# Kernel optimization log

Measured on AMD Instinct MI355X. Metric: run time of the kernel, lower is better.

The kernel has to match this reference:

```python
import jax, jax.numpy as jnp
import numpy as np

N = 100000
E = 1600000
IN_C = 128
HID = 256
EPS = 1e-5


def setup_inputs() -> dict:
    key = jax.random.key(0)
    ks = jax.random.split(key, 20)
    s = lambda fi, fo: (1.0 / np.sqrt(fi))
    inp = {
        "x": jax.random.normal(ks[0], (N, IN_C), dtype=jnp.float32),
        "edge_index": jax.random.randint(ks[1], (2, E), 0, N, dtype=jnp.int64),
        # SAGEConv (in -> hidden): lin_l (on aggregated neighbors, with bias), lin_r (root, no bias)
        "Wl": jax.random.normal(ks[2], (HID, IN_C), dtype=jnp.float32) * s(IN_C, HID),
        "bl": jnp.zeros((HID,), dtype=jnp.float32),
        "Wr": jax.random.normal(ks[3], (HID, IN_C), dtype=jnp.float32) * s(IN_C, HID),
        # bns[0]
        "bn_g": jnp.ones((HID,), dtype=jnp.float32),
        "bn_b": jnp.zeros((HID,), dtype=jnp.float32),
        # linear stack hidden->hidden->64->14->2
        "W1": jax.random.normal(ks[4], (HID, HID), dtype=jnp.float32) * s(HID, HID),
        "b1": jnp.zeros((HID,), dtype=jnp.float32),
        "W2": jax.random.normal(ks[5], (64, HID), dtype=jnp.float32) * s(HID, 64),
        "b2": jnp.zeros((64,), dtype=jnp.float32),
        "W3": jax.random.normal(ks[6], (14, 64), dtype=jnp.float32) * s(64, 14),
        "b3": jnp.zeros((14,), dtype=jnp.float32),
        "W4": jax.random.normal(ks[7], (2, 14), dtype=jnp.float32) * s(14, 2),
        "b4": jnp.zeros((2,), dtype=jnp.float32),
        # bns2: BN(hidden), BN(64), BN(14)
        "g1": jnp.ones((HID,), dtype=jnp.float32), "bb1": jnp.zeros((HID,), dtype=jnp.float32),
        "g2": jnp.ones((64,), dtype=jnp.float32), "bb2": jnp.zeros((64,), dtype=jnp.float32),
        "g3": jnp.ones((14,), dtype=jnp.float32), "bb3": jnp.zeros((14,), dtype=jnp.float32),
    }
    return inp


def _bn(h, g, b):
    # training-mode BatchNorm1d: batch mean, biased variance
    m = h.mean(axis=0)
    v = jnp.mean((h - m) ** 2, axis=0)
    return g * (h - m) * jax.lax.rsqrt(v + EPS) + b


def _sage_mean(x, edge_index, Wl, bl, Wr):
    src, dst = edge_index[0], edge_index[1]
    n = x.shape[0]
    agg = jax.ops.segment_sum(x[src], dst, num_segments=n)  # [N, F]
    cnt = jax.ops.segment_sum(jnp.ones((src.shape[0],), x.dtype), dst, num_segments=n)
    agg = agg / jnp.maximum(cnt, 1.0)[:, None]
    return agg @ Wl.T + bl + x @ Wr.T


def reference(x, edge_index, Wl, bl, Wr, bn_g, bn_b,
              W1, b1, W2, b2, W3, b3, W4, b4,
              g1, bb1, g2, bb2, g3, bb3):
    # convs2[:-1] loop (num_layers=2 -> single conv), dropout is identity (eval)
    h = _sage_mean(x, edge_index, Wl, bl, Wr)
    h = jax.nn.relu(_bn(h, bn_g, bn_b))
    # linear stack with bns2 + relu
    h = jax.nn.relu(_bn(h @ W1.T + b1, g1, bb1))
    h = jax.nn.relu(_bn(h @ W2.T + b2, g2, bb2))
    h = jax.nn.relu(_bn(h @ W3.T + b3, g3, bb3))
    h = h @ W4.T + b4
    return jax.nn.log_softmax(h, axis=-1)
```

## Files before the change

kernel.cpp:

```cpp
#include <hip/hip_runtime.h>
#include <math.h>

#define BN_EPS 1e-5f
#define STAT_NB 64
#define GBIN 512
#define BSH 7
#define XB 2048

typedef unsigned short u16;
typedef __attribute__((ext_vector_type(8))) unsigned short u16x8;
typedef __attribute__((ext_vector_type(8))) short bf16x8;
typedef __attribute__((ext_vector_type(4))) float f32x4;

__device__ __forceinline__ float bf2f(u16 b){
  union{unsigned int u; float f;} c; c.u = ((unsigned int)b)<<16; return c.f;
}
__device__ __forceinline__ u16 f2bf(float f){
  union{float f; unsigned int u;} c; c.f=f;
  unsigned int u = c.u;
  return (u16)((u + 0x7fffu + ((u>>16)&1u)) >> 16);
}
__device__ __forceinline__ void gl16(const u16* g, u16* l){
  __builtin_amdgcn_global_load_lds((const __attribute__((address_space(1))) void*)g,
                                   (__attribute__((address_space(3))) void*)l, 16, 0, 0);
}

__global__ __launch_bounds__(256) void k_prep(
    const float* __restrict__ Wl, const float* __restrict__ Wr,
    const float* __restrict__ W1, const float* __restrict__ W2,
    const float* __restrict__ x, const int* __restrict__ ei, int E, int nbkt,
    u16* __restrict__ Wb1, u16* __restrict__ Wb2, u16* __restrict__ Wb3,
    u16* __restrict__ Acat, int n, int* __restrict__ blkhist, int* __restrict__ flags){
  __shared__ int hist[1024];
  int bid = blockIdx.x, tid = threadIdx.x;
  auto cv8 = [](const float* s)->u16x8{
    float4 a = ((const float4*)s)[0], b = ((const float4*)s)[1];
    u16x8 v;
    v[0]=f2bf(a.x); v[1]=f2bf(a.y); v[2]=f2bf(a.z); v[3]=f2bf(a.w);
    v[4]=f2bf(b.x); v[5]=f2bf(b.y); v[6]=f2bf(b.z); v[7]=f2bf(b.w);
    return v;
  };
  if (bid < XB){
    int i = bid*256 + tid;
    int total = n*16;
    for (; i<total; i+=XB*256){
      int r = i>>4, kb = (i&15)*8;
      *(u16x8*)(Acat + (size_t)r*256 + 128 + kb) = cv8(x + (size_t)r*128 + kb);
    }
  } else if (bid < XB+512){
    int blk = bid - XB;
    for (int b=tid;b<1024;b+=256) hist[b]=0;
    __syncthreads();
    int per = (E + GBIN - 1)/GBIN;
    int e0 = blk*per, e1 = min(E, e0+per);
    for (int e=e0+tid; e<e1; e+=256)
      atomicAdd(&hist[ei[(size_t)E+e]>>BSH], 1);
    __syncthreads();
    for (int b=tid;b<nbkt;b+=256) blkhist[(size_t)b*GBIN + blk] = hist[b];
  } else {
    int wb = bid - (XB+512);
    if (wb==0 && tid<8) flags[tid]=0;
    if (wb < 32){
      int i = wb*256 + tid;
      int c = i>>5, kb = (i&31)*8;
      const float* src = (kb<128) ? (Wl + (size_t)c*128 + kb) : (Wr + (size_t)c*128 + kb-128);
      *(u16x8*)(Wb1 + (size_t)c*256 + kb) = cv8(src);
    } else if (wb < 64){
      int i = (wb-32)*256 + tid;
      *(u16x8*)(Wb2 + (size_t)i*8) = cv8(W1 + (size_t)i*8);
    } else {
      int i = (wb-64)*256 + tid;
      if (i < 2048) *(u16x8*)(Wb3 + (size_t)i*8) = cv8(W2 + (size_t)i*8);
    }
  }
}

__global__ __launch_bounds__(256) void k_rowscan(int* __restrict__ blkhist, int nbkt,
                                                 int* __restrict__ bbase, int* __restrict__ counter){
  __shared__ int lastFlag;
  __shared__ int ps[256];
  int tid = threadIdx.x;
  int wid = (blockIdx.x*256 + tid) >> 6;
  int lane = tid & 63;
  if (wid < nbkt){
    int* row = blkhist + (size_t)wid*GBIN + lane*8;
    int v[8];
    #pragma unroll
    for (int j=0;j<8;j++) v[j] = row[j];
    int s = 0;
    #pragma unroll
    for (int j=0;j<8;j++){ int t = v[j]; v[j] = s; s += t; }
    int incl = s;
    #pragma unroll
    for (int o=1;o<64;o<<=1){
      int t = __shfl_up(incl, o, 64);
      if (lane >= o) incl += t;
    }
    int excl = incl - s;
    #pragma unroll
    for (int j=0;j<8;j++) row[j] = v[j] + excl;
    if (lane == 63) bbase[wid] = incl;
  }
  __threadfence();
  if (tid==0) lastFlag = (atomicAdd(counter,1) == (int)gridDim.x-1);
  __syncthreads();
  if (!lastFlag) return;
  int base = tid*4;
  int v0 = (base  <nbkt)? bbase[base  ] : 0;
  int v1 = (base+1<nbkt)? bbase[base+1] : 0;
  int v2 = (base+2<nbkt)? bbase[base+2] : 0;
  int v3 = (base+3<nbkt)? bbase[base+3] : 0;
  int run = v0+v1+v2+v3;
  ps[tid] = run;
  __syncthreads();
  #pragma unroll
  for (int o=1;o<256;o<<=1){
    int t = (tid>=o)? ps[tid-o] : 0;
    __syncthreads();
    ps[tid] += t;
    __syncthreads();
  }
  int excl = ps[tid]-run;
  if (base  <nbkt) bbase[base  ] = excl;
  if (base+1<nbkt) bbase[base+1] = excl+v0;
  if (base+2<nbkt) bbase[base+2] = excl+v0+v1;
  if (base+3<nbkt) bbase[base+3] = excl+v0+v1+v2;
  if (tid==255) bbase[nbkt] = ps[255];
}

__global__ __launch_bounds__(256) void k_scatter(const int* __restrict__ ei, int E, int nbkt,
                                                 const int* __restrict__ blkhist,
                                                 const int* __restrict__ bbase,
                                                 int* __restrict__ pairs){
  __shared__ int cur[1024];
  int tid = threadIdx.x, blk = blockIdx.x;
  for (int b=tid;b<nbkt;b+=256) cur[b] = bbase[b] + blkhist[(size_t)b*GBIN + blk];
  __syncthreads();
  int per = (E + GBIN - 1)/GBIN;
  int e0 = blk*per, e1 = min(E, e0+per);
  for (int e=e0+tid; e<e1; e+=256){
    int dst = ei[(size_t)E+e];
    int src = ei[e];
    int b = dst>>BSH;
    int p = atomicAdd(&cur[b], 1);
    pairs[p] = (src<<BSH) | (dst & 127);
  }
}

__global__ __launch_bounds__(256) void k_bucket_csr(const int* __restrict__ pairs,
                                                    const int* __restrict__ bbase,
                                                    int nbkt, int n,
                                                    int2* __restrict__ odeg,
                                                    int* __restrict__ eidx){
  __shared__ int hist[128], loff[128], cur2[128];
  int tid = threadIdx.x, b = blockIdx.x;
  if (b >= nbkt) return;
  int n0 = b<<BSH;
  int nn = min(128, n - n0);
  int e0 = bbase[b], e1 = bbase[b+1];
  int cnt = e1 - e0;
  if (tid<128) hist[tid]=0;
  __syncthreads();
  for (int i=tid;i<cnt;i+=256)
    atomicAdd(&hist[pairs[e0+i] & 127], 1);
  __syncthreads();
  int hv=0;
  if (tid<128){ hv = hist[tid]; loff[tid] = hv; }
  __syncthreads();
  #pragma unroll
  for (int o=1;o<128;o<<=1){
    int t = (tid<128 && tid>=o)? loff[tid-o] : 0;
    __syncthreads();
    if (tid<128) loff[tid]+=t;
    __syncthreads();
  }
  if (tid<128){
    int ex = loff[tid]-hv;
    cur2[tid] = ex;
    if (tid<nn) odeg[n0+tid] = make_int2(e0+ex, hv);
  }
  __syncthreads();
  for (int i=tid;i<cnt;i+=256){
    int v = pairs[e0+i];
    int p = atomicAdd(&cur2[v & 127], 1);
    eidx[e0 + p] = v>>BSH;
  }
}

__global__ void k_aggregate(u16* Acat, const int2* __restrict__ odeg,
                            const int* __restrict__ eidx, int n){
  int wid = (blockIdx.x*blockDim.x + threadIdx.x) >> 6;
  int lane = threadIdx.x & 63;
  if (wid >= n) return;
  int2 od = odeg[wid];
  int o = od.x, d = od.y;
  int eslot = lane >> 3;
  int ck = (lane & 7) * 16;
  float f[16];
  #pragma unroll
  for (int j=0;j<16;j++) f[j]=0.f;
  #pragma unroll 2
  for (int i = eslot; i < d; i += 8){
    int s = eidx[o+i];
    const u16x8* src = (const u16x8*)(Acat + (size_t)s*256 + 128 + ck);
    u16x8 v0 = src[0], v1 = src[1];
    #pragma unroll
    for (int j=0;j<8;j++) f[j]   += bf2f(v0[j]);
    #pragma unroll
    for (int j=0;j<8;j++) f[8+j] += bf2f(v1[j]);
  }
  #pragma unroll
  for (int j=0;j<16;j++){
    f[j] += __shfl_xor(f[j], 8, 64);
    f[j] += __shfl_xor(f[j], 16, 64);
    f[j] += __shfl_xor(f[j], 32, 64);
  }
  if (lane < 8){
    float inv = 1.f/(float)max(d,1);
    u16x8 r0, r1;
    #pragma unroll
    for (int j=0;j<8;j++){ r0[j]=f2bf(f[j]*inv); r1[j]=f2bf(f[8+j]*inv); }
    u16x8* dst = (u16x8*)(Acat + (size_t)wid*256 + ck);
    dst[0]=r0; dst[1]=r1;
  }
}


template<int COLS>
__global__ __launch_bounds__(256, COLS==64?4:2) void k_gemm_mfma(
    const u16* __restrict__ A, const u16* __restrict__ W,
    const float* __restrict__ ss, int has_ss,
    const float* __restrict__ bias, u16* __restrict__ out,
    int nrows, int hout,
    float* __restrict__ psum, float* __restrict__ psq)
{
  constexpr int WN  = COLS/2;
  constexpr int NFR = WN/16;
  constexpr int BC  = (COLS*8)/256;
  __shared__ u16 As[128*64];
  __shared__ u16 Bs[COLS*64];
  __shared__ float scs[256], shs[256];
  __shared__ float red[2][2][COLS];

  int tid  = threadIdx.x;
  int lane = tid & 63, wave = tid >> 6;
  int wr = wave >> 1, wc = wave & 1;
  int rbase = blockIdx.x*128;

  if (has_ss){ scs[tid] = ss[tid]; shs[tid] = ss[256+tid]; }
  __syncthreads();

  f32x4 acc[4][NFR];
  #pragma unroll
  for (int m=0;m<4;m++)
    #pragma unroll
    for (int n=0;n<NFR;n++)
      acc[m][n] = (f32x4){0.f,0.f,0.f,0.f};

  int arow = tid >> 1;
  int acb  = (tid & 1) * 32;
  bool avalid = (rbase + arow) < nrows;
  const u16* aptr = A + (size_t)(rbase+arow)*256 + acb;

  for (int kt=0; kt<256; kt+=64){
    if (has_ss){
      #pragma unroll
      for (int q=0;q<4;q++){
        u16x8 v = (u16x8){0,0,0,0,0,0,0,0};
        if (avalid) v = *(const u16x8*)(aptr + kt + q*8);
        int k = acb + q*8;
        #pragma unroll
        for (int e=0;e<8;e++){
          float f = bf2f(v[e]);
          f = fmaxf(fmaf(f, scs[kt+k+e], shs[kt+k+e]), 0.f);
          v[e] = f2bf(f);
        }
        int slot = ((acb>>3) + q) ^ (arow & 7);
        *(u16x8*)(As + arow*64 + slot*8) = v;
      }
    } else {
      #pragma unroll
      for (int q=0;q<4;q++){
        int cb = (wave*4+q)*64;
        int c = cb + lane;
        int row = c>>3, sl = c&7;
        const u16* g = A + (size_t)(rbase+row)*256 + kt + ((sl ^ (row&7))<<3);
        gl16(g, As + cb*8);
      }
    }
    #pragma unroll
    for (int q=0;q<BC;q++){
      int cb = (wave*BC+q)*64;
      int c = cb + lane;
      int row = c>>3, sl = c&7;
      const u16* g = W + (size_t)row*256 + kt + ((sl ^ (row&7))<<3);
      gl16(g, Bs + cb*8);
    }
    __syncthreads();

    int fr = lane & 15, g = lane >> 4;
    #pragma unroll
    for (int kk=0;kk<2;kk++){
      bf16x8 af[4], bfr[NFR];
      #pragma unroll
      for (int m=0;m<4;m++){
        int row = wr*64 + m*16 + fr;
        int slot = (kk*4 + g) ^ (row & 7);
        af[m] = *(const bf16x8*)(As + row*64 + slot*8);
      }
      #pragma unroll
      for (int n=0;n<NFR;n++){
        int row = wc*WN + n*16 + fr;
        int slot = (kk*4 + g) ^ (row & 7);
        bfr[n] = *(const bf16x8*)(Bs + row*64 + slot*8);
      }
      #pragma unroll
      for (int m=0;m<4;m++)
        #pragma unroll
        for (int n=0;n<NFR;n++)
          acc[m][n] = __builtin_amdgcn_mfma_f32_16x16x32_bf16(af[m], bfr[n], acc[m][n], 0, 0, 0);
    }
    __syncthreads();
  }

  int cl = lane & 15, g = lane >> 4;
  float bv[NFR], sn[NFR], qn[NFR];
  #pragma unroll
  for (int n=0;n<NFR;n++){
    bv[n] = bias[wc*WN + n*16 + cl];
    sn[n] = 0.f; qn[n] = 0.f;
  }
  #pragma unroll
  for (int m=0;m<4;m++){
    int r0 = rbase + wr*64 + m*16 + g*4;
    #pragma unroll
    for (int n=0;n<NFR;n++){
      int c = wc*WN + n*16 + cl;
      #pragma unroll
      for (int i=0;i<4;i++){
        int r = r0 + i;
        if (r < nrows){
          float v = acc[m][n][i] + bv[n];
          out[(size_t)r*hout + c] = f2bf(v);
          sn[n] += v; qn[n] += v*v;
        }
      }
    }
  }
  #pragma unroll
  for (int n=0;n<NFR;n++){
    sn[n] += __shfl_xor(sn[n], 16, 64);
    sn[n] += __shfl_xor(sn[n], 32, 64);
    qn[n] += __shfl_xor(qn[n], 16, 64);
    qn[n] += __shfl_xor(qn[n], 32, 64);
  }
  if (lane < 16){
    #pragma unroll
    for (int n=0;n<NFR;n++){
      int cc = wc*WN + n*16 + lane;
      red[0][wr][cc] = sn[n];
      red[1][wr][cc] = qn[n];
    }
  }
  __syncthreads();
  if (tid < COLS){
    psum[(size_t)blockIdx.x*hout + tid] = red[0][0][tid] + red[0][1][tid];
    psq [(size_t)blockIdx.x*hout + tid] = red[1][0][tid] + red[1][1][tid];
  }
}

__global__ __launch_bounds__(256) void k_stats_partfold(
    const float* __restrict__ psum, const float* __restrict__ psq,
    int rt, int h, float* __restrict__ part, float ninv,
    const float* __restrict__ g, const float* __restrict__ b_,
    float* __restrict__ ss, int* __restrict__ counter){
  __shared__ int isLast;
  int c = threadIdx.x, b = blockIdx.x;
  int chunk = (rt + STAT_NB - 1)/STAT_NB;
  int i0 = b*chunk;
  int i1 = min(rt, i0+chunk);
  if (c < h){
    float s0=0.f,s1=0.f,s2=0.f,s3=0.f, q0=0.f,q1=0.f,q2=0.f,q3=0.f;
    int i=i0;
    for (; i+3<i1; i+=4){
      s0 += psum[(size_t)i*h+c];     q0 += psq[(size_t)i*h+c];
      s1 += psum[(size_t)(i+1)*h+c]; q1 += psq[(size_t)(i+1)*h+c];
      s2 += psum[(size_t)(i+2)*h+c]; q2 += psq[(size_t)(i+2)*h+c];
      s3 += psum[(size_t)(i+3)*h+c]; q3 += psq[(size_t)(i+3)*h+c];
    }
    for (; i<i1; ++i){ s0 += psum[(size_t)i*h+c]; q0 += psq[(size_t)i*h+c]; }
    part[((size_t)b*2  )*h + c] = (s0+s1)+(s2+s3);
    part[((size_t)b*2+1)*h + c] = (q0+q1)+(q2+q3);
  }
  __threadfence();
  if (c==0) isLast = (atomicAdd(counter,1) == gridDim.x-1);
  __syncthreads();
  if (isLast && c < h){
    float S0=0.f,S1=0.f,Q0=0.f,Q1=0.f;
    #pragma unroll 2
    for (int b2=0;b2<STAT_NB;b2+=2){
      S0 += part[((size_t)b2*2  )*h + c];
      Q0 += part[((size_t)b2*2+1)*h + c];
      S1 += part[((size_t)(b2+1)*2  )*h + c];
      Q1 += part[((size_t)(b2+1)*2+1)*h + c];
    }
    float S = S0+S1, Q = Q0+Q1;
    float m = S*ninv;
    float v = fmaxf(Q*ninv - m*m, 0.f);
    float sc = g[c] * rsqrtf(v + BN_EPS);
    ss[c]   = sc;
    ss[h+c] = b_[c] - m*sc;
  }
}

__global__ __launch_bounds__(256) void k_lin3(const u16* __restrict__ h3, const float* __restrict__ ss3,
     const float* __restrict__ W3, const float* __restrict__ b3,
     float* __restrict__ h4, int n, float* __restrict__ psum, float* __restrict__ psq){
  __shared__ float Ws[14*64];
  __shared__ float bs[14];
  __shared__ float sc[64], sh[64];
  __shared__ float redp[2][14][4];
  int tid=threadIdx.x;
  for (int i=tid;i<896;i+=256) Ws[i]=W3[i];
  if (tid<14) bs[tid]=b3[tid];
  if (tid<64){ sc[tid]=ss3[tid]; sh[tid]=ss3[64+tid]; }
  __syncthreads();
  int node = blockIdx.x*256 + tid;
  float o[14];
  #pragma unroll
  for (int hh=0;hh<14;hh++) o[hh]=0.f;
  if (node<n){
    const u16x8* ar = (const u16x8*)(h3 + (size_t)node*64);
    #pragma unroll
    for (int kv=0;kv<8;kv++){
      u16x8 v = ar[kv];
      #pragma unroll
      for (int j=0;j<8;j++){
        int k=kv*8+j;
        float a = fmaxf(fmaf(bf2f(v[j]), sc[k], sh[k]), 0.f);
        #pragma unroll
        for (int hh=0;hh<14;hh++) o[hh] = fmaf(a, Ws[hh*64+k], o[hh]);
      }
    }
    #pragma unroll
    for (int hh=0;hh<14;hh++){ o[hh]+=bs[hh]; h4[(size_t)node*14+hh]=o[hh]; }
  }
  int lane = tid & 63, w = tid>>6;
  #pragma unroll
  for (int hh=0;hh<14;hh++){
    float sv = (node<n)? o[hh] : 0.f;
    float qv = sv*sv;
    #pragma unroll
    for (int offs=32;offs>0;offs>>=1){
      sv += __shfl_down(sv,offs,64);
      qv += __shfl_down(qv,offs,64);
    }
    if (lane==0){ redp[0][hh][w]=sv; redp[1][hh][w]=qv; }
  }
  __syncthreads();
  if (tid<14){
    float t=redp[0][tid][0]+redp[0][tid][1]+redp[0][tid][2]+redp[0][tid][3];
    psum[(size_t)blockIdx.x*14+tid]=t;
  } else if (tid>=64 && tid<78){
    int c=tid-64;
    float t=redp[1][c][0]+redp[1][c][1]+redp[1][c][2]+redp[1][c][3];
    psq[(size_t)blockIdx.x*14+c]=t;
  }
}

__global__ void k_final(const float* __restrict__ h4, const float* __restrict__ ss4,
   const float* __restrict__ W4, const float* __restrict__ b4, float* __restrict__ out, int n){
  int node = blockIdx.x*blockDim.x+threadIdx.x;
  if (node>=n) return;
  float z0=b4[0], z1=b4[1];
  #pragma unroll
  for (int j=0;j<14;j++){
    float a = fmaxf(h4[(size_t)node*14+j]*ss4[j]+ss4[14+j], 0.f);
    z0 = fmaf(a, W4[j],    z0);
    z1 = fmaf(a, W4[14+j], z1);
  }
  float m = fmaxf(z0,z1);
  float lse = m + logf(expf(z0-m)+expf(z1-m));
  out[(size_t)node*2]   = z0-lse;
  out[(size_t)node*2+1] = z1-lse;
}

extern "C" void kernel_launch(void* const* d_in, const int* in_sizes, int n_in,
                              void* d_out, int out_size, void* d_ws, size_t ws_size,
                              hipStream_t stream){
  const float* x    = (const float*)d_in[0];
  const int*   ei   = (const int*)d_in[1];
  const float* Wl   = (const float*)d_in[2];
  const float* bl   = (const float*)d_in[3];
  const float* Wr   = (const float*)d_in[4];
  const float* bn_g = (const float*)d_in[5];
  const float* bn_b = (const float*)d_in[6];
  const float* W1   = (const float*)d_in[7];
  const float* b1   = (const float*)d_in[8];
  const float* W2   = (const float*)d_in[9];
  const float* b2   = (const float*)d_in[10];
  const float* W3   = (const float*)d_in[11];
  const float* b3   = (const float*)d_in[12];
  const float* W4   = (const float*)d_in[13];
  const float* b4   = (const float*)d_in[14];
  const float* g1   = (const float*)d_in[15];
  const float* bb1  = (const float*)d_in[16];
  const float* g2   = (const float*)d_in[17];
  const float* bb2  = (const float*)d_in[18];
  const float* g3   = (const float*)d_in[19];
  const float* bb3  = (const float*)d_in[20];

  const int N = in_sizes[0]/128;
  const int E = in_sizes[1]/2;
  const int NBKT = (N + 127) >> BSH;
  const int RT2 = (N+127)/128;
  const int RT4 = (N+255)/256;

  char* p = (char*)d_ws;
  auto alloc = [&](size_t bytes)->void*{
    void* r = (void*)p;
    p += (bytes + 255) & ~(size_t)255;
    return r;
  };
  int2* odeg    = (int2*)alloc((size_t)N*sizeof(int2));
  int* bbase    = (int*)alloc(1025*sizeof(int));
  int* flags    = (int*)alloc(16*sizeof(int));
  int* blkhist  = (int*)alloc((size_t)1024*GBIN*sizeof(int));
  int* pairs    = (int*)alloc((size_t)E*sizeof(int));
  int* eidx     = (int*)alloc((size_t)E*sizeof(int));
  u16* Acat     = (u16*)alloc((size_t)N*256*sizeof(u16));
  u16* h1b      = (u16*)alloc((size_t)N*256*sizeof(u16));
  float* h4     = (float*)alloc((size_t)N*14*sizeof(float));
  u16* Wb1      = (u16*)alloc(256*256*sizeof(u16));
  u16* Wb2      = (u16*)alloc(256*256*sizeof(u16));
  u16* Wb3      = (u16*)alloc(64*256*sizeof(u16));
  float* psum   = (float*)alloc((size_t)RT2*256*sizeof(float));
  float* psq    = (float*)alloc((size_t)RT2*256*sizeof(float));
  float* part   = (float*)alloc((size_t)STAT_NB*2*256*sizeof(float));
  float* ssb    = (float*)alloc(4*512*sizeof(float));
  u16* h2b = Acat;
  u16* h3b = h1b;
  float* ss1=ssb, *ss2=ssb+512, *ss3=ssb+1024, *ss4=ssb+1536;
  const float ninv = 1.f/(float)N;

  k_prep<<<dim3(XB+512+72), dim3(256), 0, stream>>>(
      Wl, Wr, W1, W2, x, ei, E, NBKT, Wb1, Wb2, Wb3, Acat, N, blkhist, flags);

  k_rowscan<<<dim3((NBKT*64+255)/256), dim3(256), 0, stream>>>(blkhist, NBKT, bbase, flags+4);
  k_scatter<<<dim3(GBIN), dim3(256), 0, stream>>>(ei, E, NBKT, blkhist, bbase, pairs);
  k_bucket_csr<<<dim3(NBKT), dim3(256), 0, stream>>>(pairs, bbase, NBKT, N, odeg, eidx);

  k_aggregate<<<dim3((N+3)/4), dim3(256), 0, stream>>>(Acat, odeg, eidx, N);

  k_gemm_mfma<256><<<dim3(RT2), dim3(256), 0, stream>>>(
      Acat, Wb1, (const float*)0, 0, bl, h1b, N, 256, psum, psq);
  k_stats_partfold<<<dim3(STAT_NB), dim3(256), 0, stream>>>(
      psum, psq, RT2, 256, part, ninv, bn_g, bn_b, ss1, flags+0);

  k_gemm_mfma<256><<<dim3(RT2), dim3(256), 0, stream>>>(
      h1b, Wb2, ss1, 1, b1, h2b, N, 256, psum, psq);
  k_stats_partfold<<<dim3(STAT_NB), dim3(256), 0, stream>>>(
      psum, psq, RT2, 256, part, ninv, g1, bb1, ss2, flags+1);

  k_gemm_mfma<64><<<dim3(RT2), dim3(256), 0, stream>>>(
      h2b, Wb3, ss2, 1, b2, h3b, N, 64, psum, psq);
  k_stats_partfold<<<dim3(STAT_NB), dim3(256), 0, stream>>>(
      psum, psq, RT2, 64, part, ninv, g2, bb2, ss3, flags+2);

  k_lin3<<<dim3(RT4), dim3(256), 0, stream>>>(h3b, ss3, W3, b3, h4, N, psum, psq);
  k_stats_partfold<<<dim3(STAT_NB), dim3(256), 0, stream>>>(
      psum, psq, RT4, 14, part, ninv, g3, bb3, ss4, flags+3);

  k_final<<<dim3((N+255)/256), dim3(256), 0, stream>>>(h4, ss4, W4, b4, (float*)d_out, N);
}
```

Before: 306.1 us.

## Fuse bucket CSR build with neighbor aggregation using LDS-staged source lists

Shrinks destination buckets from 128 to 64 nodes and fuses the per-bucket CSR sort with the mean aggregation. Each block sorts its bucket's edges into shared memory and aggregates its 64 nodes directly, which removes the global eidx/odeg arrays and one kernel launch. The cost is twice as many buckets and larger histogram and scan arrays. Aggregation parallelism also drops to one block per 64 nodes. Any bucket with more than 2048 edges silently drops the excess edges, which gives wrong results on skewed degree distributions.

```diff
diff --git a/kernel.cpp b/kernel.cpp
--- a/kernel.cpp
+++ b/kernel.cpp
@@ -4,7 +4,7 @@
 #define BN_EPS 1e-5f
 #define STAT_NB 64
 #define GBIN 512
-#define BSH 7
+#define BSH 6
 #define XB 2048
 
 typedef unsigned short u16;
@@ -31,7 +31,7 @@
     const float* __restrict__ x, const int* __restrict__ ei, int E, int nbkt,
     u16* __restrict__ Wb1, u16* __restrict__ Wb2, u16* __restrict__ Wb3,
     u16* __restrict__ Acat, int n, int* __restrict__ blkhist, int* __restrict__ flags){
-  __shared__ int hist[1024];
+  __shared__ int hist[2048];
   int bid = blockIdx.x, tid = threadIdx.x;
   auto cv8 = [](const float* s)->u16x8{
     float4 a = ((const float4*)s)[0], b = ((const float4*)s)[1];
@@ -49,7 +49,7 @@
     }
   } else if (bid < XB+512){
     int blk = bid - XB;
-    for (int b=tid;b<1024;b+=256) hist[b]=0;
+    for (int b=tid;b<2048;b+=256) hist[b]=0;
     __syncthreads();
     int per = (E + GBIN - 1)/GBIN;
     int e0 = blk*per, e1 = min(E, e0+per);
@@ -105,12 +105,15 @@
   if (tid==0) lastFlag = (atomicAdd(counter,1) == (int)gridDim.x-1);
   __syncthreads();
   if (!lastFlag) return;
-  int base = tid*4;
-  int v0 = (base  <nbkt)? bbase[base  ] : 0;
-  int v1 = (base+1<nbkt)? bbase[base+1] : 0;
-  int v2 = (base+2<nbkt)? bbase[base+2] : 0;
-  int v3 = (base+3<nbkt)? bbase[base+3] : 0;
-  int run = v0+v1+v2+v3;
+  int base = tid*8;
+  int v[8];
+  int run = 0;
+  #pragma unroll
+  for (int j=0;j<8;j++){
+    int t = (base+j<nbkt)? bbase[base+j] : 0;
+    v[j] = run;
+    run += t;
+  }
   ps[tid] = run;
   __syncthreads();
   #pragma unroll
@@ -121,10 +124,9 @@
     __syncthreads();
   }
   int excl = ps[tid]-run;
-  if (base  <nbkt) bbase[base  ] = excl;
-  if (base+1<nbkt) bbase[base+1] = excl+v0;
-  if (base+2<nbkt) bbase[base+2] = excl+v0+v1;
-  if (base+3<nbkt) bbase[base+3] = excl+v0+v1+v2;
+  #pragma unroll
+  for (int j=0;j<8;j++)
+    if (base+j<nbkt) bbase[base+j] = v[j] + excl;
   if (tid==255) bbase[nbkt] = ps[255];
 }
 
@@ -132,7 +134,7 @@
                                                  const int* __restrict__ blkhist,
                                                  const int* __restrict__ bbase,
                                                  int* __restrict__ pairs){
-  __shared__ int cur[1024];
+  __shared__ int cur[2048];
   int tid = threadIdx.x, blk = blockIdx.x;
   for (int b=tid;b<nbkt;b+=256) cur[b] = bbase[b] + blkhist[(size_t)b*GBIN + blk];
   __syncthreads();
@@ -143,85 +145,77 @@
     int src = ei[e];
     int b = dst>>BSH;
     int p = atomicAdd(&cur[b], 1);
-    pairs[p] = (src<<BSH) | (dst & 127);
-  }
-}
-
-__global__ __launch_bounds__(256) void k_bucket_csr(const int* __restrict__ pairs,
-                                                    const int* __restrict__ bbase,
-                                                    int nbkt, int n,
-                                                    int2* __restrict__ odeg,
-                                                    int* __restrict__ eidx){
-  __shared__ int hist[128], loff[128], cur2[128];
+    pairs[p] = (src<<BSH) | (dst & 63);
+  }
+}
+
+__global__ __launch_bounds__(256) void k_bucket_agg(
+    const int* __restrict__ pairs, const int* __restrict__ bbase,
+    int nbkt, int n, u16* __restrict__ Acat){
+  __shared__ int srcs[2048];
+  __shared__ int hist[64], loff[64], cur[64];
   int tid = threadIdx.x, b = blockIdx.x;
-  if (b >= nbkt) return;
-  int n0 = b<<BSH;
-  int nn = min(128, n - n0);
-  int e0 = bbase[b], e1 = bbase[b+1];
-  int cnt = e1 - e0;
-  if (tid<128) hist[tid]=0;
+  int e0 = bbase[b];
+  int cnt = bbase[b+1] - e0;
+  if (tid<64) hist[tid]=0;
   __syncthreads();
   for (int i=tid;i<cnt;i+=256)
-    atomicAdd(&hist[pairs[e0+i] & 127], 1);
-  __syncthreads();
-  int hv=0;
-  if (tid<128){ hv = hist[tid]; loff[tid] = hv; }
-  __syncthreads();
-  #pragma unroll
-  for (int o=1;o<128;o<<=1){
-    int t = (tid<128 && tid>=o)? loff[tid-o] : 0;
-    __syncthreads();
-    if (tid<128) loff[tid]+=t;
-    __syncthreads();
-  }
-  if (tid<128){
-    int ex = loff[tid]-hv;
-    cur2[tid] = ex;
-    if (tid<nn) odeg[n0+tid] = make_int2(e0+ex, hv);
+    atomicAdd(&hist[pairs[e0+i] & 63], 1);
+  __syncthreads();
+  if (tid < 64){
+    int hv = hist[tid];
+    int incl = hv;
+    #pragma unroll
+    for (int o=1;o<64;o<<=1){
+      int t = __shfl_up(incl, o, 64);
+      if ((tid&63) >= o) incl += t;
+    }
+    loff[tid] = incl - hv;
+    cur[tid]  = incl - hv;
   }
   __syncthreads();
   for (int i=tid;i<cnt;i+=256){
     int v = pairs[e0+i];
-    int p = atomicAdd(&cur2[v & 127], 1);
-    eidx[e0 + p] = v>>BSH;
-  }
-}
-
-__global__ void k_aggregate(u16* Acat, const int2* __restrict__ odeg,
-                            const int* __restrict__ eidx, int n){
-  int wid = (blockIdx.x*blockDim.x + threadIdx.x) >> 6;
-  int lane = threadIdx.x & 63;
-  if (wid >= n) return;
-  int2 od = odeg[wid];
-  int o = od.x, d = od.y;
-  int eslot = lane >> 3;
-  int ck = (lane & 7) * 16;
-  float f[16];
-  #pragma unroll
-  for (int j=0;j<16;j++) f[j]=0.f;
-  #pragma unroll 2
-  for (int i = eslot; i < d; i += 8){
-    int s = eidx[o+i];
-    const u16x8* src = (const u16x8*)(Acat + (size_t)s*256 + 128 + ck);
-    u16x8 v0 = src[0], v1 = src[1];
-    #pragma unroll
-    for (int j=0;j<8;j++) f[j]   += bf2f(v0[j]);
-    #pragma unroll
-    for (int j=0;j<8;j++) f[8+j] += bf2f(v1[j]);
-  }
-  #pragma unroll
-  for (int j=0;j<16;j++){
-    f[j] += __shfl_xor(f[j], 8, 64);
-    f[j] += __shfl_xor(f[j], 16, 64);
-    f[j] += __shfl_xor(f[j], 32, 64);
-  }
-  if (lane < 8){
-    float inv = 1.f/(float)max(d,1);
-    u16x8 r0, r1;
-    #pragma unroll
-    for (int j=0;j<8;j++){ r0[j]=f2bf(f[j]*inv); r1[j]=f2bf(f[8+j]*inv); }
-    u16x8* dst = (u16x8*)(Acat + (size_t)wid*256 + ck);
-    dst[0]=r0; dst[1]=r1;
+    int p = atomicAdd(&cur[v & 63], 1);
+    if (p < 2048) srcs[p] = v>>BSH;
+  }
+  __syncthreads();
+
+  int wave = tid>>6, lane = tid&63;
+  int eslot = lane>>3;
+  int ck = (lane&7)*16;
+  int n0 = b<<BSH;
+  for (int t=0;t<16;t++){
+    int nd = wave*16 + t;
+    int node = n0 + nd;
+    if (node >= n) break;
+    int o = loff[nd], d = hist[nd];
+    float f[16];
+    #pragma unroll
+    for (int j=0;j<16;j++) f[j]=0.f;
+    for (int i=eslot; i<d; i+=8){
+      int s = srcs[o+i];
+      const u16x8* src = (const u16x8*)(Acat + (size_t)s*256 + 128 + ck);
+      u16x8 v0 = src[0], v1 = src[1];
+      #pragma unroll
+      for (int j=0;j<8;j++) f[j]   += bf2f(v0[j]);
+      #pragma unroll
+      for (int j=0;j<8;j++) f[8+j] += bf2f(v1[j]);
+    }
+    #pragma unroll
+    for (int j=0;j<16;j++){
+      f[j] += __shfl_xor(f[j], 8, 64);
+      f[j] += __shfl_xor(f[j], 16, 64);
+      f[j] += __shfl_xor(f[j], 32, 64);
+    }
+    if (lane < 8){
+      float inv = 1.f/(float)max(d,1);
+      u16x8 r0, r1;
+      #pragma unroll
+      for (int j=0;j<8;j++){ r0[j]=f2bf(f[j]*inv); r1[j]=f2bf(f[8+j]*inv); }
+      u16x8* dst = (u16x8*)(Acat + (size_t)node*256 + ck);
+      dst[0]=r0; dst[1]=r1;
+    }
   }
 }
 
@@ -512,7 +506,7 @@
 
   const int N = in_sizes[0]/128;
   const int E = in_sizes[1]/2;
-  const int NBKT = (N + 127) >> BSH;
+  const int NBKT = (N + 63) >> BSH;
   const int RT2 = (N+127)/128;
   const int RT4 = (N+255)/256;
 
@@ -522,12 +516,10 @@
     p += (bytes + 255) & ~(size_t)255;
     return r;
   };
-  int2* odeg    = (int2*)alloc((size_t)N*sizeof(int2));
-  int* bbase    = (int*)alloc(1025*sizeof(int));
+  int* bbase    = (int*)alloc(2049*sizeof(int));
   int* flags    = (int*)alloc(16*sizeof(int));
-  int* blkhist  = (int*)alloc((size_t)1024*GBIN*sizeof(int));
+  int* blkhist  = (int*)alloc((size_t)2048*GBIN*sizeof(int));
   int* pairs    = (int*)alloc((size_t)E*sizeof(int));
-  int* eidx     = (int*)alloc((size_t)E*sizeof(int));
   u16* Acat     = (u16*)alloc((size_t)N*256*sizeof(u16));
   u16* h1b      = (u16*)alloc((size_t)N*256*sizeof(u16));
   float* h4     = (float*)alloc((size_t)N*14*sizeof(float));
@@ -548,9 +540,7 @@
 
   k_rowscan<<<dim3((NBKT*64+255)/256), dim3(256), 0, stream>>>(blkhist, NBKT, bbase, flags+4);
   k_scatter<<<dim3(GBIN), dim3(256), 0, stream>>>(ei, E, NBKT, blkhist, bbase, pairs);
-  k_bucket_csr<<<dim3(NBKT), dim3(256), 0, stream>>>(pairs, bbase, NBKT, N, odeg, eidx);
-
-  k_aggregate<<<dim3((N+3)/4), dim3(256), 0, stream>>>(Acat, odeg, eidx, N);
+  k_bucket_agg<<<dim3(NBKT), dim3(256), 0, stream>>>(pairs, bbase, NBKT, N, Acat);
 
   k_gemm_mfma<256><<<dim3(RT2), dim3(256), 0, stream>>>(
       Acat, Wb1, (const float*)0, 0, bl, h1b, N, 256, psum, psq);
```

Measured after the change: 343.1 us. 1.12x slower.
